# Kernel tuning notes

Hardware: AMD Instinct MI355X
Metric: run time of the kernel (lower is better)

## Reference

```python
import jax, jax.numpy as jnp
import numpy as np

B, C, H, W = 32, 384, 56, 56
SPARSE = 8
HEADS = 8
HIDDEN = 4 * C
EPS = 1e-5


def _ln(x, g, b):
    m = jnp.mean(x, axis=-1, keepdims=True)
    v = jnp.mean((x - m) ** 2, axis=-1, keepdims=True)
    return (x - m) * jax.lax.rsqrt(v + EPS) * g + b


def setup_inputs() -> dict:
    key = jax.random.key(0)
    ks = jax.random.split(key, 12)
    s = 0.02
    return {
        "x": jax.random.normal(ks[0], (B, C, H, W), jnp.float32),
        "ln1_g": jnp.ones((C,), jnp.float32),
        "ln1_b": jnp.zeros((C,), jnp.float32),
        "qkv_w": jax.random.normal(ks[1], (C, 3 * C), jnp.float32) * s,
        "proj_w": jax.random.normal(ks[2], (C, C), jnp.float32) * s,
        "proj_b": jnp.zeros((C,), jnp.float32),
        "ln2_g": jnp.ones((C,), jnp.float32),
        "ln2_b": jnp.zeros((C,), jnp.float32),
        "fc1_w": jax.random.normal(ks[3], (C, HIDDEN), jnp.float32) * s,
        "fc1_b": jnp.zeros((HIDDEN,), jnp.float32),
        "dw_w": jax.random.normal(ks[4], (HIDDEN, 1, 3, 3), jnp.float32) * np.sqrt(2.0 / 9.0),
        "dw_b": jnp.zeros((HIDDEN,), jnp.float32),
        "fc2_w": jax.random.normal(ks[5], (HIDDEN, C), jnp.float32) * s,
        "fc2_b": jnp.zeros((C,), jnp.float32),
        "gamma1": jnp.full((C,), 1e-6, jnp.float32),
        "gamma2": jnp.full((C,), 1e-6, jnp.float32),
    }


def reference(x, ln1_g, ln1_b, qkv_w, proj_w, proj_b, ln2_g, ln2_b,
              fc1_w, fc1_b, dw_w, dw_b, fc2_w, fc2_b, gamma1, gamma2):
    Bx, Cx, Hx, Wx = x.shape
    s = SPARSE
    g = Hx // s  # grid size; H divisible by sparse_size per module assert
    N = Hx * Wx
    hd = Cx // HEADS
    scale = hd ** (-0.5)

    x_before = x.reshape(Bx, Cx, N).transpose(0, 2, 1)  # [B,N,C]

    # alter_sparse: gather tokens spaced g apart into s x s windows
    xw = x.transpose(0, 2, 3, 1).reshape(Bx, s, g, s, g, Cx)
    xw = xw.transpose(0, 2, 4, 1, 3, 5).reshape(Bx * g * g, s * s, Cx)

    # attention on windows
    h = _ln(xw, ln1_g, ln1_b)
    qkv = (h @ qkv_w).reshape(Bx * g * g, s * s, 3, HEADS, hd)
    q, k, v = (qkv[:, :, i].transpose(0, 2, 1, 3) for i in range(3))  # [Bw,h,n,d]
    attn = jax.nn.softmax(jnp.einsum('bhqd,bhkd->bhqk', q, k) * scale, axis=-1)
    o = jnp.einsum('bhqk,bhkd->bhqd', attn, v).transpose(0, 2, 1, 3)
    o = o.reshape(Bx * g * g, s * s, Cx) @ proj_w + proj_b

    # alter_unsparse: scatter windows back to spatial layout
    o = o.reshape(Bx, g, g, s, s, Cx).transpose(0, 3, 1, 4, 2, 5)
    o = o.reshape(Bx, Hx, Wx, Cx).reshape(Bx, N, Cx)

    x1 = x_before + gamma1 * o

    # MLP with depthwise conv
    m = _ln(x1, ln2_g, ln2_b) @ fc1_w + fc1_b  # [B,N,hidden]
    m2 = m.transpose(0, 2, 1).reshape(Bx, HIDDEN, Hx, Wx)
    m2 = jax.lax.conv_general_dilated(
        m2, dw_w, window_strides=(1, 1), padding=((1, 1), (1, 1)),
        dimension_numbers=('NCHW', 'OIHW', 'NCHW'),
        feature_group_count=HIDDEN) + dw_b[None, :, None, None]
    m = m2.reshape(Bx, HIDDEN, N).transpose(0, 2, 1)
    m = jax.nn.gelu(m, approximate=False)
    m = m @ fc2_w + fc2_b

    x2 = x1 + gamma2 * m
    return x2.transpose(0, 2, 1).reshape(Bx, Cx, Hx, Wx)
```

## Files before the change

kernel.cpp:

```cpp
#include <hip/hip_runtime.h>
#include <hip/hip_bf16.h>

typedef __hip_bfloat16 bf16;
typedef float v4f __attribute__((ext_vector_type(4)));
typedef __attribute__((ext_vector_type(8))) short short8;

__device__ __forceinline__ float b2f(bf16 v) { return __bfloat162float(v); }
__device__ __forceinline__ bf16 f2b(float v) { return __float2bfloat16(v); }

__device__ __forceinline__ void gload_lds16(const bf16* g, bf16* l) {
    __builtin_amdgcn_global_load_lds((__attribute__((address_space(1))) void*)(void*)g,
                                     (__attribute__((address_space(3))) void*)l, 16, 0, 0);
}

#define BB 32
#define CD 384
#define HH 56
#define ND 3136
#define HID 1536
#define GG 7
#define SS 8
#define MROWS 100352

__device__ __forceinline__ int wrow_to_token(int orow) {
    int w = orow >> 6, t = orow & 63;
    int bb = w / 49, wr = w % 49;
    int gy = wr / GG, gx = wr % GG;
    int sy = t >> 3, sx = t & 7;
    return bb * ND + (sy * GG + gy) * HH + (sx * GG + gx);
}

__global__ __launch_bounds__(256) void transpose_f2b_k(const float* __restrict__ in,
                                                       bf16* __restrict__ out, int R, int Cc)
{
    __shared__ float tile[32][33];
    int c0 = blockIdx.x * 32, r0 = blockIdx.y * 32;
    size_t bb = blockIdx.z;
    int tx = threadIdx.x & 31, ty = threadIdx.x >> 5;
    const float* ip = in + bb * (size_t)R * Cc;
    bf16* op = out + bb * (size_t)R * Cc;
#pragma unroll
    for (int i = 0; i < 4; i++)
        tile[ty + i * 8][tx] = ip[(size_t)(r0 + ty + i * 8) * Cc + (c0 + tx)];
    __syncthreads();
#pragma unroll
    for (int i = 0; i < 4; i++)
        op[(size_t)(c0 + ty + i * 8) * R + (r0 + tx)] = f2b(tile[tx][ty + i * 8]);
}

__global__ __launch_bounds__(256) void ln_k(const bf16* __restrict__ in,
                                            const float* __restrict__ g,
                                            const float* __restrict__ b,
                                            bf16* __restrict__ out,
                                            int row0, int gather)
{
    int wave = threadIdx.x >> 6, lane = threadIdx.x & 63;
    int row = row0 + blockIdx.x * 4 + wave;
    int src = gather ? wrow_to_token(row) : row;
    const bf16* ip = in + (size_t)src * CD;
    float vals[6];
    float s = 0.f, s2 = 0.f;
#pragma unroll
    for (int i = 0; i < 6; i++) {
        float v = b2f(ip[lane + i * 64]);
        vals[i] = v; s += v; s2 += v * v;
    }
#pragma unroll
    for (int off = 32; off >= 1; off >>= 1) {
        s  += __shfl_xor(s, off);
        s2 += __shfl_xor(s2, off);
    }
    float mean = s * (1.f / CD);
    float var = s2 * (1.f / CD) - mean * mean;
    float rstd = rsqrtf(var + 1e-5f);
    bf16* op = out + (size_t)(row - row0) * CD;
#pragma unroll
    for (int i = 0; i < 6; i++) {
        int c = lane + i * 64;
        op[c] = f2b((vals[i] - mean) * rstd * g[c] + b[c]);
    }
}

__global__ __launch_bounds__(256) void gemm_bt(const bf16* __restrict__ A,
                                               const bf16* __restrict__ Bt,
                                               const float* __restrict__ bias,
                                               bf16* __restrict__ Cm,
                                               int M, int N, int K)
{
    __shared__ __align__(16) bf16 As[128][32];
    __shared__ __align__(16) bf16 Bs[128][32];
    const int tid = threadIdx.x;
    const int m0 = blockIdx.y * 128, n0 = blockIdx.x * 128;
    const int lane = tid & 63, wave = tid >> 6;
    const int rb = (wave >> 1) * 64, cb = (wave & 1) * 64;
    const int lr = lane & 15, ko = (lane >> 4) * 8;
    const int srow = lane >> 2;
    const int scol = (lane & 3) * 8;

    v4f acc[4][4];
#pragma unroll
    for (int i = 0; i < 4; i++)
#pragma unroll
        for (int j = 0; j < 4; j++) acc[i][j] = (v4f)0.f;

    for (int kk = 0; kk < K; kk += 32) {
        const int r0 = wave * 32;
#pragma unroll
        for (int h = 0; h < 2; h++) {
            int row = r0 + h * 16 + srow;
            gload_lds16(&A [(size_t)(m0 + row) * K + kk + scol], &As[r0 + h * 16][0]);
            gload_lds16(&Bt[(size_t)(n0 + row) * K + kk + scol], &Bs[r0 + h * 16][0]);
        }
        __syncthreads();
        short8 af[4], bfr[4];
#pragma unroll
        for (int mi = 0; mi < 4; mi++) af[mi]  = *(const short8*)&As[rb + mi * 16 + lr][ko];
#pragma unroll
        for (int ni = 0; ni < 4; ni++) bfr[ni] = *(const short8*)&Bs[cb + ni * 16 + lr][ko];
#pragma unroll
        for (int mi = 0; mi < 4; mi++)
#pragma unroll
            for (int ni = 0; ni < 4; ni++)
                acc[mi][ni] = __builtin_amdgcn_mfma_f32_16x16x32_bf16(af[mi], bfr[ni], acc[mi][ni], 0, 0, 0);
        __syncthreads();
    }
#pragma unroll
    for (int ni = 0; ni < 4; ni++) {
        int col = n0 + cb + ni * 16 + lr;
        float bv = bias ? bias[col] : 0.f;
#pragma unroll
        for (int mi = 0; mi < 4; mi++) {
            int rowb = m0 + rb + mi * 16 + (lane >> 4) * 4;
#pragma unroll
            for (int r = 0; r < 4; r++)
                Cm[(size_t)(rowb + r) * N + col] = f2b(acc[mi][ni][r] + bv);
        }
    }
}

__global__ __launch_bounds__(64) void attn_mfma_k(const bf16* __restrict__ qkv,
                                                  bf16* __restrict__ o)
{
    __shared__ __align__(16) char lds[20480];
    bf16* Qs = (bf16*)lds;
    bf16* Ks = (bf16*)(lds + 7168);
    bf16* Vs = (bf16*)(lds + 14336);
    char* Ps = lds;

    const int lane = threadIdx.x;
    const int lr = lane & 15, grp = lane >> 4;
    const int lw = blockIdx.x >> 3, head = blockIdx.x & 7;

    const bf16* base = qkv + (size_t)lw * 64 * 1152 + head * 48;

#pragma unroll
    for (int it = 0; it < 7; it++) {
        int i = it * 64 + lane;
        int t = i / 7, s = i - t * 7;
        uint4 zq = {0, 0, 0, 0}, zk = {0, 0, 0, 0};
        if (s < 6) {
            const bf16* p = base + (size_t)t * 1152 + s * 8;
            zq = *(const uint4*)p;
            zk = *(const uint4*)(p + 384);
        }
        *(uint4*)((char*)Qs + t * 112 + s * 16) = zq;
        *(uint4*)((char*)Ks + t * 112 + s * 16) = zk;
    }
#pragma unroll
    for (int it = 0; it < 6; it++) {
        int i = it * 64 + lane;
        int t = i / 6, s = i - t * 6;
        *(uint4*)((char*)Vs + t * 96 + s * 16) =
            *(const uint4*)(base + (size_t)t * 1152 + 768 + s * 8);
    }

    v4f accs[4][4];
#pragma unroll
    for (int mi = 0; mi < 4; mi++)
#pragma unroll
        for (int ni = 0; ni < 4; ni++) accs[mi][ni] = (v4f)0.f;

    {
        short8 qf[4], kf[4];
#pragma unroll
        for (int mi = 0; mi < 4; mi++)
            qf[mi] = *(const short8*)((char*)Qs + (mi * 16 + lr) * 112 + grp * 16);
#pragma unroll
        for (int ni = 0; ni < 4; ni++)
            kf[ni] = *(const short8*)((char*)Ks + (ni * 16 + lr) * 112 + grp * 16);
#pragma unroll
        for (int mi = 0; mi < 4; mi++)
#pragma unroll
            for (int ni = 0; ni < 4; ni++)
                accs[mi][ni] = __builtin_amdgcn_mfma_f32_16x16x32_bf16(qf[mi], kf[ni], accs[mi][ni], 0, 0, 0);
        int koff2 = (grp < 2) ? (64 + grp * 16) : 96;
#pragma unroll
        for (int mi = 0; mi < 4; mi++)
            qf[mi] = *(const short8*)((char*)Qs + (mi * 16 + lr) * 112 + koff2);
#pragma unroll
        for (int ni = 0; ni < 4; ni++)
            kf[ni] = *(const short8*)((char*)Ks + (ni * 16 + lr) * 112 + koff2);
#pragma unroll
        for (int mi = 0; mi < 4; mi++)
#pragma unroll
            for (int ni = 0; ni < 4; ni++)
                accs[mi][ni] = __builtin_amdgcn_mfma_f32_16x16x32_bf16(qf[mi], kf[ni], accs[mi][ni], 0, 0, 0);
    }

    const float scale = 0.14433756729740643f;
#pragma unroll
    for (int mi = 0; mi < 4; mi++)
#pragma unroll
        for (int ni = 0; ni < 4; ni++) accs[mi][ni] *= scale;

    float inv_s[4][4];
#pragma unroll
    for (int mi = 0; mi < 4; mi++) {
#pragma unroll
        for (int r = 0; r < 4; r++) {
            float mx = fmaxf(fmaxf(accs[mi][0][r], accs[mi][1][r]),
                             fmaxf(accs[mi][2][r], accs[mi][3][r]));
#pragma unroll
            for (int off = 8; off >= 1; off >>= 1) mx = fmaxf(mx, __shfl_xor(mx, off));
            float sum = 0.f;
#pragma unroll
            for (int ni = 0; ni < 4; ni++) {
                float e = __expf(accs[mi][ni][r] - mx);
                accs[mi][ni][r] = e;
                sum += e;
            }
#pragma unroll
            for (int off = 8; off >= 1; off >>= 1) sum += __shfl_xor(sum, off);
            inv_s[mi][r] = 1.f / sum;
        }
    }

#pragma unroll
    for (int mi = 0; mi < 4; mi++)
#pragma unroll
        for (int ni = 0; ni < 4; ni++)
#pragma unroll
            for (int r = 0; r < 4; r++) {
                int i = mi * 16 + grp * 4 + r;
                int j = ni * 16 + lr;
                int byte = (i * 128 + j * 2) ^ ((i & 7) << 4);
                *(bf16*)(Ps + byte) = f2b(accs[mi][ni][r]);
            }

    v4f acco[4][3];
#pragma unroll
    for (int mi = 0; mi < 4; mi++)
#pragma unroll
        for (int ni = 0; ni < 3; ni++) acco[mi][ni] = (v4f)0.f;

    const short* vsp = (const short*)Vs;
#pragma unroll
    for (int kk = 0; kk < 2; kk++) {
        int k0 = kk * 32 + grp * 8;
        short8 pf[4];
#pragma unroll
        for (int mi = 0; mi < 4; mi++) {
            int row = mi * 16 + lr;
            int byte = (row * 128 + k0 * 2) ^ ((row & 7) << 4);
            pf[mi] = *(const short8*)(Ps + byte);
        }
        short8 vf[3];
#pragma unroll
        for (int ni = 0; ni < 3; ni++) {
#pragma unroll
            for (int jj = 0; jj < 8; jj++)
                vf[ni][jj] = vsp[(k0 + jj) * 48 + ni * 16 + lr];
        }
#pragma unroll
        for (int mi = 0; mi < 4; mi++)
#pragma unroll
            for (int ni = 0; ni < 3; ni++)
                acco[mi][ni] = __builtin_amdgcn_mfma_f32_16x16x32_bf16(pf[mi], vf[ni], acco[mi][ni], 0, 0, 0);
    }

    bf16* op = o + (size_t)lw * 64 * CD + head * 48;
#pragma unroll
    for (int mi = 0; mi < 4; mi++)
#pragma unroll
        for (int r = 0; r < 4; r++) {
            int t = mi * 16 + grp * 4 + r;
            float is = inv_s[mi][r];
#pragma unroll
            for (int ni = 0; ni < 3; ni++)
                op[(size_t)t * CD + ni * 16 + lr] = f2b(acco[mi][ni][r] * is);
        }
}

__global__ __launch_bounds__(256) void resid1_k(const bf16* __restrict__ xt,
                                                const bf16* __restrict__ oprojc,
                                                const float* __restrict__ gamma1,
                                                bf16* __restrict__ x1, int row0)
{
    int idx = blockIdx.x * 256 + threadIdx.x;
    int lrow = idx / CD, c = idx % CD;
    int token = wrow_to_token(row0 + lrow);
    size_t xi = (size_t)token * CD + c;
    x1[xi] = f2b(b2f(xt[xi]) + gamma1[c] * b2f(oprojc[idx]));
}

__global__ __launch_bounds__(256) void dwconv_gelu_k(const bf16* __restrict__ m1c,
                                                     const float* __restrict__ wgt,
                                                     const float* __restrict__ bias,
                                                     bf16* __restrict__ gc)
{
    const int c  = blockIdx.x * 64 + (threadIdx.x & 63);
    const int xq = threadIdx.x >> 6;
    const int xx = blockIdx.y * 8 + xq * 2;
    const int lb = blockIdx.z >> 2;
    const int ys = (blockIdx.z & 3) * 14;

    float w9[9];
#pragma unroll
    for (int i = 0; i < 9; i++) w9[i] = wgt[c * 9 + i];
    const float bs = bias[c];

    const bf16* base = m1c + (size_t)lb * ND * HID + c;
    bool  v[4];
    const bf16* colp[4];
#pragma unroll
    for (int i = 0; i < 4; i++) {
        int xc = xx - 1 + i;
        v[i] = (xc >= 0 && xc < HH);
        int xcl = xc < 0 ? 0 : (xc > HH - 1 ? HH - 1 : xc);
        colp[i] = base + (size_t)xcl * HID;
    }
    const size_t ystride = (size_t)HH * HID;

    float win[3][4];
    {
        int ym = ys - 1;
        int ymc = ym < 0 ? 0 : ym;
        bool yv = (ym >= 0);
#pragma unroll
        for (int i = 0; i < 4; i++)
            win[0][i] = (yv && v[i]) ? b2f(colp[i][(size_t)ymc * ystride]) : 0.f;
#pragma unroll
        for (int i = 0; i < 4; i++)
            win[1][i] = v[i] ? b2f(colp[i][(size_t)ys * ystride]) : 0.f;
    }

#pragma unroll
    for (int s = 0; s < 14; s++) {
        const int y = ys + s;
        const int yp = y + 1;
        const bool yv = (yp < HH);
        const int ypc = yv ? yp : (HH - 1);
#pragma unroll
        for (int i = 0; i < 4; i++)
            win[2][i] = (yv && v[i]) ? b2f(colp[i][(size_t)ypc * ystride]) : 0.f;

        float a0 = bs, a1 = bs;
#pragma unroll
        for (int r = 0; r < 3; r++)
#pragma unroll
            for (int j = 0; j < 3; j++) {
                a0 = fmaf(w9[r * 3 + j], win[r][j],     a0);
                a1 = fmaf(w9[r * 3 + j], win[r][j + 1], a1);
            }
        float g0 = 0.5f * a0 * (1.f + erff(a0 * 0.70710678118654752f));
        float g1 = 0.5f * a1 * (1.f + erff(a1 * 0.70710678118654752f));
        size_t o0 = ((size_t)lb * ND + (size_t)y * HH + xx) * HID + c;
        gc[o0]       = f2b(g0);
        gc[o0 + HID] = f2b(g1);

#pragma unroll
        for (int i = 0; i < 4; i++) { win[0][i] = win[1][i]; win[1][i] = win[2][i]; }
    }
}

__global__ __launch_bounds__(256) void resid2_k(const bf16* __restrict__ x1,
                                                const bf16* __restrict__ m2c,
                                                const float* __restrict__ gamma2,
                                                float* __restrict__ out, int b0)
{
    __shared__ float tile[32][33];
    int n0 = blockIdx.x * 32, c0 = blockIdx.y * 32;
    int lb = blockIdx.z, gb = b0 + lb;
    int tx = threadIdx.x & 31, ty = threadIdx.x >> 5;
#pragma unroll
    for (int i = 0; i < 4; i++) {
        int n = n0 + ty + i * 8, c = c0 + tx;
        size_t sx1 = ((size_t)gb * ND + n) * CD + c;
        size_t sm  = ((size_t)lb * ND + n) * CD + c;
        tile[ty + i * 8][tx] = b2f(x1[sx1]) + gamma2[c] * b2f(m2c[sm]);
    }
    __syncthreads();
#pragma unroll
    for (int i = 0; i < 4; i++) {
        int c = c0 + ty + i * 8, n = n0 + tx;
        out[((size_t)gb * CD + c) * ND + n] = tile[tx][ty + i * 8];
    }
}

extern "C" void kernel_launch(void* const* d_in, const int* in_sizes, int n_in,
                              void* d_out, int out_size, void* d_ws, size_t ws_size,
                              hipStream_t stream) {
    const float* x      = (const float*)d_in[0];
    const float* ln1_g  = (const float*)d_in[1];
    const float* ln1_b  = (const float*)d_in[2];
    const float* qkv_w  = (const float*)d_in[3];
    const float* proj_w = (const float*)d_in[4];
    const float* proj_b = (const float*)d_in[5];
    const float* ln2_g  = (const float*)d_in[6];
    const float* ln2_b  = (const float*)d_in[7];
    const float* fc1_w  = (const float*)d_in[8];
    const float* fc1_b  = (const float*)d_in[9];
    const float* dw_w   = (const float*)d_in[10];
    const float* dw_b   = (const float*)d_in[11];
    const float* fc2_w  = (const float*)d_in[12];
    const float* fc2_b  = (const float*)d_in[13];
    const float* gamma1 = (const float*)d_in[14];
    const float* gamma2 = (const float*)d_in[15];
    float* out = (float*)d_out;

    const size_t SZ_TOK = (size_t)MROWS * CD * 2;
    const size_t S0 = 2 * SZ_TOK;
    const size_t WTS = 3538944;

    const size_t attn_end8 = S0 + (size_t)(MROWS / 8) * CD * 2 + (size_t)(MROWS / 8) * 1152 * 2;
    int cm = 16;
    {
        size_t mc2 = (size_t)(BB / 8) * ND;
        size_t mlp_end8 = S0 + mc2 * CD * 2 + 2 * mc2 * HID * 2;
        size_t tot8 = (mlp_end8 > attn_end8 ? mlp_end8 : attn_end8) + WTS;
        if (ws_size >= tot8) cm = 8;
    }
    const int nb = BB / cm;
    const int Mc2 = nb * ND;
    const size_t sz_h2 = (size_t)Mc2 * CD * 2;
    const size_t sz_m1 = (size_t)Mc2 * HID * 2;
    const size_t mlp_end = S0 + sz_h2 + 2 * sz_m1;

    int ca = 0;
    size_t sz_h = 0, sz_qk = 0, attn_end = 0;
    for (int cand = 2; cand <= 8 && !ca; cand <<= 1) {
        int McA_ = MROWS / cand;
        size_t h_ = (size_t)McA_ * CD * 2, qk_ = (size_t)McA_ * 1152 * 2;
        size_t ae = S0 + h_ + qk_;
        size_t tot = (mlp_end > ae ? mlp_end : ae) + WTS;
        if (ws_size >= tot) { ca = cand; sz_h = h_; sz_qk = qk_; attn_end = ae; }
    }
    if (!ca) return;
    const int McA = MROWS / ca;

    const size_t Wo = (mlp_end > attn_end ? mlp_end : attn_end);

    char* w = (char*)d_ws;
    bf16* xt      = (bf16*)(w + 0);
    bf16* x1      = (bf16*)(w + SZ_TOK);
    bf16* hc      = (bf16*)(w + S0);
    bf16* qkvc    = (bf16*)(w + S0 + sz_h);
    bf16* h2c     = (bf16*)(w + S0);
    bf16* m1c     = (bf16*)(w + S0 + sz_h2);
    bf16* gc      = (bf16*)(w + S0 + sz_h2 + sz_m1);
    bf16* qkv_wt  = (bf16*)(w + Wo);
    bf16* proj_wt = (bf16*)(w + Wo + 884736);
    bf16* fc1_wt  = (bf16*)(w + Wo + 884736 + 294912);
    bf16* fc2_wt  = (bf16*)(w + Wo + 884736 + 294912 + 1179648);

    dim3 blk(256);

    transpose_f2b_k<<<dim3(98, 12, 32), blk, 0, stream>>>(x, xt, CD, ND);
    transpose_f2b_k<<<dim3(36, 12, 1), blk, 0, stream>>>(qkv_w, qkv_wt, CD, 1152);
    transpose_f2b_k<<<dim3(12, 12, 1), blk, 0, stream>>>(proj_w, proj_wt, CD, CD);
    transpose_f2b_k<<<dim3(48, 12, 1), blk, 0, stream>>>(fc1_w, fc1_wt, CD, HID);
    transpose_f2b_k<<<dim3(12, 48, 1), blk, 0, stream>>>(fc2_w, fc2_wt, HID, CD);

    for (int ch = 0; ch < ca; ch++) {
        int row0 = ch * McA;
        ln_k<<<McA / 4, blk, 0, stream>>>(xt, ln1_g, ln1_b, hc, row0, 1);
        gemm_bt<<<dim3(9, McA / 128), blk, 0, stream>>>(hc, qkv_wt, nullptr, qkvc, McA, 1152, CD);
        attn_mfma_k<<<(McA / 64) * 8, dim3(64), 0, stream>>>(qkvc, hc);
        gemm_bt<<<dim3(3, McA / 128), blk, 0, stream>>>(hc, proj_wt, proj_b, qkvc, McA, CD, CD);
        resid1_k<<<(McA * CD) / 256, blk, 0, stream>>>(xt, qkvc, gamma1, x1, row0);
    }

    for (int ch = 0; ch < cm; ch++) {
        int r0 = ch * Mc2, b0 = ch * nb;
        ln_k<<<Mc2 / 4, blk, 0, stream>>>(x1, ln2_g, ln2_b, h2c, r0, 0);
        gemm_bt<<<dim3(12, Mc2 / 128), blk, 0, stream>>>(h2c, fc1_wt, fc1_b, m1c, Mc2, HID, CD);
        dwconv_gelu_k<<<dim3(HID / 64, 7, nb * 4), blk, 0, stream>>>(m1c, dw_w, dw_b, gc);
        gemm_bt<<<dim3(3, Mc2 / 128), blk, 0, stream>>>(gc, fc2_wt, fc2_b, h2c, Mc2, CD, HID);
        resid2_k<<<dim3(98, 12, nb), blk, 0, stream>>>(x1, h2c, gamma2, out, b0);
    }
}
```

Measured before the change: 1.835 ms.

## Remap GEMM workgroups across XCDs and load Q/K fragments directly from global

The GEMM launch becomes a 1D grid, and each block's ID is remapped so consecutive tiles land on the same XCD. Neighbouring tiles then share that XCD's L2 cache for A and B reuse. Separately, the attention kernel no longer stages Q and K through LDS. It reads the MFMA operand fragments straight from global memory, zero-filling the padded tail of K, which shrinks LDS use and drops a staging pass. The trade-off is that the global reads for Q/K fragments are strided and less coalesced.

```diff
diff --git a/kernel.cpp b/kernel.cpp
--- a/kernel.cpp
+++ b/kernel.cpp
@@ -85,12 +85,17 @@
                                                const bf16* __restrict__ Bt,
                                                const float* __restrict__ bias,
                                                bf16* __restrict__ Cm,
-                                               int M, int N, int K)
+                                               int M, int N, int K, int gx)
 {
     __shared__ __align__(16) bf16 As[128][32];
     __shared__ __align__(16) bf16 Bs[128][32];
+    const int nwg = gridDim.x;
+    const int q = nwg >> 3, r = nwg & 7;
+    const int xcd = blockIdx.x & 7, id8 = blockIdx.x >> 3;
+    const int wgid = (xcd < r ? xcd * (q + 1) : r * (q + 1) + (xcd - r) * q) + id8;
+    const int m0 = (wgid / gx) * 128, n0 = (wgid % gx) * 128;
+
     const int tid = threadIdx.x;
-    const int m0 = blockIdx.y * 128, n0 = blockIdx.x * 128;
     const int lane = tid & 63, wave = tid >> 6;
     const int rb = (wave >> 1) * 64, cb = (wave & 1) * 64;
     const int lr = lane & 15, ko = (lane >> 4) * 8;
@@ -141,11 +146,9 @@
 __global__ __launch_bounds__(64) void attn_mfma_k(const bf16* __restrict__ qkv,
                                                   bf16* __restrict__ o)
 {
-    __shared__ __align__(16) char lds[20480];
-    bf16* Qs = (bf16*)lds;
-    bf16* Ks = (bf16*)(lds + 7168);
-    bf16* Vs = (bf16*)(lds + 14336);
+    __shared__ __align__(16) char lds[14336];
     char* Ps = lds;
+    bf16* Vs = (bf16*)(lds + 8192);
 
     const int lane = threadIdx.x;
     const int lr = lane & 15, grp = lane >> 4;
@@ -153,19 +156,6 @@
 
     const bf16* base = qkv + (size_t)lw * 64 * 1152 + head * 48;
 
-#pragma unroll
-    for (int it = 0; it < 7; it++) {
-        int i = it * 64 + lane;
-        int t = i / 7, s = i - t * 7;
-        uint4 zq = {0, 0, 0, 0}, zk = {0, 0, 0, 0};
-        if (s < 6) {
-            const bf16* p = base + (size_t)t * 1152 + s * 8;
-            zq = *(const uint4*)p;
-            zk = *(const uint4*)(p + 384);
-        }
-        *(uint4*)((char*)Qs + t * 112 + s * 16) = zq;
-        *(uint4*)((char*)Ks + t * 112 + s * 16) = zk;
-    }
 #pragma unroll
     for (int it = 0; it < 6; it++) {
         int i = it * 64 + lane;
@@ -180,26 +170,26 @@
 #pragma unroll
         for (int ni = 0; ni < 4; ni++) accs[mi][ni] = (v4f)0.f;
 
+    const short8 z8 = (short8)0;
     {
         short8 qf[4], kf[4];
 #pragma unroll
         for (int mi = 0; mi < 4; mi++)
-            qf[mi] = *(const short8*)((char*)Qs + (mi * 16 + lr) * 112 + grp * 16);
+            qf[mi] = *(const short8*)(base + (size_t)(mi * 16 + lr) * 1152 + grp * 8);
 #pragma unroll
         for (int ni = 0; ni < 4; ni++)
-            kf[ni] = *(const short8*)((char*)Ks + (ni * 16 + lr) * 112 + grp * 16);
+            kf[ni] = *(const short8*)(base + 384 + (size_t)(ni * 16 + lr) * 1152 + grp * 8);
 #pragma unroll
         for (int mi = 0; mi < 4; mi++)
 #pragma unroll
             for (int ni = 0; ni < 4; ni++)
                 accs[mi][ni] = __builtin_amdgcn_mfma_f32_16x16x32_bf16(qf[mi], kf[ni], accs[mi][ni], 0, 0, 0);
-        int koff2 = (grp < 2) ? (64 + grp * 16) : 96;
-#pragma unroll
-        for (int mi = 0; mi < 4; mi++)
-            qf[mi] = *(const short8*)((char*)Qs + (mi * 16 + lr) * 112 + koff2);
+#pragma unroll
+        for (int mi = 0; mi < 4; mi++)
+            qf[mi] = (grp < 2) ? *(const short8*)(base + (size_t)(mi * 16 + lr) * 1152 + 32 + grp * 8) : z8;
 #pragma unroll
         for (int ni = 0; ni < 4; ni++)
-            kf[ni] = *(const short8*)((char*)Ks + (ni * 16 + lr) * 112 + koff2);
+            kf[ni] = (grp < 2) ? *(const short8*)(base + 384 + (size_t)(ni * 16 + lr) * 1152 + 32 + grp * 8) : z8;
 #pragma unroll
         for (int mi = 0; mi < 4; mi++)
 #pragma unroll
@@ -474,18 +464,18 @@
     for (int ch = 0; ch < ca; ch++) {
         int row0 = ch * McA;
         ln_k<<<McA / 4, blk, 0, stream>>>(xt, ln1_g, ln1_b, hc, row0, 1);
-        gemm_bt<<<dim3(9, McA / 128), blk, 0, stream>>>(hc, qkv_wt, nullptr, qkvc, McA, 1152, CD);
+        gemm_bt<<<dim3(9 * (McA / 128)), blk, 0, stream>>>(hc, qkv_wt, nullptr, qkvc, McA, 1152, CD, 9);
         attn_mfma_k<<<(McA / 64) * 8, dim3(64), 0, stream>>>(qkvc, hc);
-        gemm_bt<<<dim3(3, McA / 128), blk, 0, stream>>>(hc, proj_wt, proj_b, qkvc, McA, CD, CD);
+        gemm_bt<<<dim3(3 * (McA / 128)), blk, 0, stream>>>(hc, proj_wt, proj_b, qkvc, McA, CD, CD, 3);
         resid1_k<<<(McA * CD) / 256, blk, 0, stream>>>(xt, qkvc, gamma1, x1, row0);
     }
 
     for (int ch = 0; ch < cm; ch++) {
         int r0 = ch * Mc2, b0 = ch * nb;
         ln_k<<<Mc2 / 4, blk, 0, stream>>>(x1, ln2_g, ln2_b, h2c, r0, 0);
-        gemm_bt<<<dim3(12, Mc2 / 128), blk, 0, stream>>>(h2c, fc1_wt, fc1_b, m1c, Mc2, HID, CD);
+        gemm_bt<<<dim3(12 * (Mc2 / 128)), blk, 0, stream>>>(h2c, fc1_wt, fc1_b, m1c, Mc2, HID, CD, 12);
         dwconv_gelu_k<<<dim3(HID / 64, 7, nb * 4), blk, 0, stream>>>(m1c, dw_w, dw_b, gc);
-        gemm_bt<<<dim3(3, Mc2 / 128), blk, 0, stream>>>(gc, fc2_wt, fc2_b, h2c, Mc2, CD, HID);
+        gemm_bt<<<dim3(3 * (Mc2 / 128)), blk, 0, stream>>>(gc, fc2_wt, fc2_b, h2c, Mc2, CD, HID, 3);
         resid2_k<<<dim3(98, 12, nb), blk, 0, stream>>>(x1, h2c, gamma2, out, b0);
     }
 }
```

New measurement: 1.784 ms. 2.8% less time.
